# Optimization experiments

Measured on AMD Instinct MI355X. Metric: run time of the kernel, lower is better.

## Reference

```python
import jax, jax.numpy as jnp
import numpy as np

EMBED_DIM = 1024
HEAD_DIM = 128

def setup_inputs() -> dict:
    key = jax.random.key(0)
    ks = jax.random.split(key, 7)
    B, S = 4, 2048
    x = jax.random.normal(ks[0], (B, S, EMBED_DIM), dtype=jnp.float32)
    # Linear params: weight [embed_dim, head_dim] (applied as x @ W + b), scaled init
    scale = 1.0 / np.sqrt(EMBED_DIM)
    Wq = jax.random.normal(ks[1], (EMBED_DIM, HEAD_DIM), dtype=jnp.float32) * scale
    Wk = jax.random.normal(ks[2], (EMBED_DIM, HEAD_DIM), dtype=jnp.float32) * scale
    Wv = jax.random.normal(ks[3], (EMBED_DIM, HEAD_DIM), dtype=jnp.float32) * scale
    bq = jax.random.normal(ks[4], (HEAD_DIM,), dtype=jnp.float32) * 0.01
    bk = jax.random.normal(ks[5], (HEAD_DIM,), dtype=jnp.float32) * 0.01
    bv = jax.random.normal(ks[6], (HEAD_DIM,), dtype=jnp.float32) * 0.01
    return {"x": x, "Wq": Wq, "bq": bq, "Wk": Wk, "bk": bk, "Wv": Wv, "bv": bv}

def reference(x, Wq, bq, Wk, bk, Wv, bv):
    # x: [B, S, E]
    S = x.shape[1]
    norm = jnp.asarray(HEAD_DIM ** 0.5, x.dtype)
    q = x @ Wq + bq  # [B, S, D]
    k = x @ Wk + bk
    v = x @ Wv + bv
    scores = jnp.einsum('bsd,btd->bst', q, k) / norm  # [B, S, S]
    causal = jnp.tril(jnp.ones((S, S), dtype=bool))
    scores = jnp.where(causal, scores, -jnp.inf)
    att = jax.nn.softmax(scores, axis=-1)
    return jnp.einsum('bst,btd->bsd', att, v)  # [B, S, D]
```

## Files before the change

kernel.cpp:

```cpp
#include <hip/hip_runtime.h>
#include <hip/hip_bf16.h>

typedef __attribute__((ext_vector_type(8))) short short8;
typedef __attribute__((ext_vector_type(4))) float f32x4;

static __device__ __forceinline__ unsigned short f2bf(float f){
  union { float f; unsigned int u; } v; v.f = f;
  unsigned int r = v.u + 0x7fffu + ((v.u >> 16) & 1u);
  return (unsigned short)(r >> 16);
}

static __device__ __forceinline__ void load_lds16(const unsigned short* g, unsigned short* l){
  __builtin_amdgcn_global_load_lds(
      (const __attribute__((address_space(1))) unsigned int*)(g),
      (__attribute__((address_space(3))) unsigned int*)(l), 16, 0, 0);
}

__global__ void k_cvt_x(const float* __restrict__ x, unsigned short* __restrict__ xb){
  int i = (blockIdx.x * 256 + threadIdx.x) * 8;
  float4 a = *(const float4*)(x + i);
  float4 b = *(const float4*)(x + i + 4);
  unsigned short h[8];
  h[0]=f2bf(a.x); h[1]=f2bf(a.y); h[2]=f2bf(a.z); h[3]=f2bf(a.w);
  h[4]=f2bf(b.x); h[5]=f2bf(b.y); h[6]=f2bf(b.z); h[7]=f2bf(b.w);
  *(uint4*)(xb + i) = *(uint4*)h;
}

__global__ void k_prep_w(const float* __restrict__ Wq, const float* __restrict__ Wk,
                         const float* __restrict__ Wv,
                         const float* __restrict__ bq, const float* __restrict__ bk,
                         const float* __restrict__ bv,
                         unsigned short* __restrict__ Wt, float* __restrict__ bias){
  int gid = blockIdx.x * 256 + threadIdx.x;
  int p = gid >> 17;
  int rem = gid & 131071;
  int d = rem >> 10, e = rem & 1023;
  const float* W = (p==0) ? Wq : ((p==1) ? Wk : Wv);
  Wt[gid] = f2bf(W[e*128 + d]);
  if (gid < 384){
    int pp = gid >> 7, dd = gid & 127;
    bias[gid] = (pp==0) ? bq[dd] : ((pp==1) ? bk[dd] : bv[dd]);
  }
}

__global__ __launch_bounds__(256) void k_gemm_qkv(
    const unsigned short* __restrict__ Xb, const unsigned short* __restrict__ Wt,
    float* __restrict__ Cp){
  __shared__ __align__(16) unsigned short As[128*64];
  __shared__ __align__(16) unsigned short Bs[128*64];
  int tid = threadIdx.x;
  int m0 = blockIdx.x * 128;
  int p  = blockIdx.y;
  int kh = blockIdx.z;
  int w = tid >> 6, lane = tid & 63, quad = lane >> 4, l16 = lane & 15;
  int wm = (w >> 1) * 64, wn = (w & 1) * 64;
  f32x4 acc[4][4];
  #pragma unroll
  for (int i=0;i<4;i++)
    #pragma unroll
    for (int j=0;j<4;j++) acc[i][j] = (f32x4){0.f,0.f,0.f,0.f};

  const unsigned short* Wp = Wt + p * (128*1024);
  int rowbase = w * 32;
  const unsigned short* Ag = Xb + (m0 + rowbase + (lane>>3))*1024 + (lane&7)*8;
  const unsigned short* Bg = Wp + (rowbase + (lane>>3))*1024 + (lane&7)*8;
  unsigned short* Al = As + rowbase*64;
  unsigned short* Bl = Bs + rowbase*64;

  int kbeg = kh*512, kend = kbeg + 512;
  for (int k0 = kbeg; k0 < kend; k0 += 64){
    #pragma unroll
    for (int s8=0; s8<4; s8++){
      load_lds16(Ag + k0 + s8*8192, Al + s8*512);
      load_lds16(Bg + k0 + s8*8192, Bl + s8*512);
    }
    __syncthreads();
    #pragma unroll
    for (int kk=0; kk<64; kk+=32){
      short8 af[4], bf[4];
      #pragma unroll
      for (int i=0;i<4;i++) af[i] = *(const short8*)(As + (wm + i*16 + l16)*64 + kk + quad*8);
      #pragma unroll
      for (int j=0;j<4;j++) bf[j] = *(const short8*)(Bs + (wn + j*16 + l16)*64 + kk + quad*8);
      #pragma unroll
      for (int i=0;i<4;i++)
        #pragma unroll
        for (int j=0;j<4;j++)
          acc[i][j] = __builtin_amdgcn_mfma_f32_16x16x32_bf16(af[i], bf[j], acc[i][j], 0,0,0);
    }
    __syncthreads();
  }
  float* slot = Cp + (size_t)(((p*64 + blockIdx.x)*2 + kh)) * 16384;
  #pragma unroll
  for (int i=0;i<4;i++)
    #pragma unroll
    for (int j=0;j<4;j++)
      #pragma unroll
      for (int r=0;r<4;r++)
        slot[(wm + i*16 + quad*4 + r)*128 + wn + j*16 + l16] = acc[i][j][r];
}

__global__ __launch_bounds__(256) void k_gcomb(const float* __restrict__ Cp,
    const float* __restrict__ bias,
    unsigned short* __restrict__ Qsw, unsigned short* __restrict__ Ksw,
    unsigned short* __restrict__ Vsw){
  int mt = blockIdx.x, p = blockIdx.y, tid = threadIdx.x;
  const float* c0p = Cp + (size_t)((p*64+mt)*2) * 16384;
  const float* c1p = c0p + 16384;
  int m0 = mt*128;
  const float qscale = 0.08838834764831845f;
  if (p < 2){
    unsigned short* dst = (p==0)? Qsw : Ksw;
    float scale = (p==0)? qscale : 1.0f;
    for (int it=0; it<16; it++){
      int g = it*256 + tid;
      int row = g >> 5, cs = (g & 31)*4;
      f32x4 a = *(const f32x4*)(c0p + row*128 + cs);
      f32x4 bb = *(const f32x4*)(c1p + row*128 + cs);
      int grow = m0 + row;
      int rt = grow >> 4, m = grow & 15;
      int kc = cs >> 5, q2 = (cs >> 3) & 3, jj = cs & 7;
      unsigned short pk[4];
      #pragma unroll
      for (int k=0;k<4;k++) pk[k] = f2bf((a[k]+bb[k]+bias[p*128+cs+k])*scale);
      *(uint2*)(dst + rt*2048 + kc*512 + q2*128 + m*8 + jj) = *(uint2*)pk;
    }
  } else {
    for (int it=0; it<16; it++){
      int g = it*256 + tid;
      int col = g & 127, rg = g >> 7;
      int r0 = rg*4;
      float bv_ = bias[256 + col];
      unsigned short pk[4];
      #pragma unroll
      for (int k=0;k<4;k++){
        int row = r0 + k;
        pk[k] = f2bf(c0p[row*128+col] + c1p[row*128+col] + bv_);
      }
      int grow0 = m0 + r0;
      int bb2 = grow0 >> 11, s = grow0 & 2047;
      int t64 = s >> 6, srem = s & 63;
      int kc2 = srem >> 5, q2 = (srem >> 3) & 3, jj = srem & 7;
      int nt = col >> 4, l2 = col & 15;
      *(uint2*)(Vsw + (bb2*32+t64)*8192 + nt*1024 + kc2*512 + q2*128 + l2*8 + jj) = *(uint2*)pk;
    }
  }
}

__global__ __launch_bounds__(64) void k_attn(
    const unsigned short* __restrict__ Qsw, const unsigned short* __restrict__ Ksw,
    const unsigned short* __restrict__ Vsw, float* __restrict__ Apart){
  __shared__ __align__(16) unsigned short Pw[2*16*80];
  int x = blockIdx.x;
  int b = x & 3;
  int t = x >> 2;
  int c = t & 7;
  int qb = 63 - (t >> 3);
  int T32 = (qb >> 1) + 1;
  int nch = (T32 + 3) >> 2;
  if (c >= nch) return;
  int lane = threadIdx.x;
  int quad = lane >> 4, l16 = lane & 15;
  int q0 = qb * 32;

  short8 aq[2][4];
  #pragma unroll
  for (int s=0;s<2;s++)
    #pragma unroll
    for (int kc=0;kc<4;kc++)
      aq[s][kc] = *(const short8*)(Qsw + (b*128 + qb*2 + s)*2048 + kc*512 + lane*8);

  f32x4 o[2][8];
  #pragma unroll
  for (int s=0;s<2;s++)
    #pragma unroll
    for (int i=0;i<8;i++) o[s][i] = (f32x4){0.f,0.f,0.f,0.f};
  float mcol[2] = {-1e30f,-1e30f};
  float lcol[2] = {0.f,0.f};
  short8 ap[2][2];

  const unsigned short* Kb = Ksw + b*128*2048;
  const unsigned short* Vb = Vsw + b*32*8192;

  int tEnd = (T32 < c*4+4) ? T32 : (c*4+4);
  for (int tt = c*4; tt < tEnd; tt++){
    int t0 = tt * 64;
    f32x4 sc[2][4];
    #pragma unroll
    for (int s=0;s<2;s++)
      #pragma unroll
      for (int nt=0;nt<4;nt++) sc[s][nt] = (f32x4){0.f,0.f,0.f,0.f};
    #pragma unroll
    for (int nt=0;nt<4;nt++){
      const unsigned short* Kt = Kb + ((t0>>4)+nt)*2048 + lane*8;
      #pragma unroll
      for (int kc=0;kc<4;kc++){
        short8 kf = *(const short8*)(Kt + kc*512);
        sc[0][nt] = __builtin_amdgcn_mfma_f32_16x16x32_bf16(kf, aq[0][kc], sc[0][nt], 0,0,0);
        sc[1][nt] = __builtin_amdgcn_mfma_f32_16x16x32_bf16(kf, aq[1][kc], sc[1][nt], 0,0,0);
      }
    }
    #pragma unroll
    for (int s=0;s<2;s++){
      int qs = q0 + s*16;
      if (t0 + 63 > qs){
        #pragma unroll
        for (int nt=0;nt<4;nt++){
          int kb_ = t0 + nt*16 + quad*4;
          #pragma unroll
          for (int r=0;r<4;r++)
            if (kb_ + r > qs + l16) sc[s][nt][r] = -1e30f;
        }
      }
      float mt_ = -1e30f;
      #pragma unroll
      for (int nt=0;nt<4;nt++)
        #pragma unroll
        for (int r=0;r<4;r++) mt_ = fmaxf(mt_, sc[s][nt][r]);
      mt_ = fmaxf(mt_, __shfl_xor(mt_, 16));
      mt_ = fmaxf(mt_, __shfl_xor(mt_, 32));
      float mn = fmaxf(mcol[s], mt_);
      float al = __expf(mcol[s] - mn);
      mcol[s] = mn;
      float ls = 0.f;
      #pragma unroll
      for (int nt=0;nt<4;nt++)
        #pragma unroll
        for (int r=0;r<4;r++){
          float pv = __expf(sc[s][nt][r] - mn);
          sc[s][nt][r] = pv;
          ls += pv;
        }
      ls += __shfl_xor(ls, 16);
      ls += __shfl_xor(ls, 32);
      lcol[s] = lcol[s]*al + ls;
      #pragma unroll
      for (int r=0;r<4;r++){
        float ar = __shfl(al, quad*4 + r);
        #pragma unroll
        for (int nt=0;nt<8;nt++) o[s][nt][r] *= ar;
      }
      unsigned short* Pws = Pw + s*1280;
      #pragma unroll
      for (int nt=0;nt<4;nt++){
        unsigned short pk[4];
        #pragma unroll
        for (int r=0;r<4;r++) pk[r] = f2bf(sc[s][nt][r]);
        *(uint2*)(Pws + l16*80 + nt*16 + quad*4) = *(uint2*)pk;
      }
      ap[s][0] = *(const short8*)(Pws + l16*80 + quad*8);
      ap[s][1] = *(const short8*)(Pws + l16*80 + 32 + quad*8);
    }
    const unsigned short* Vt0 = Vb + (t0>>6)*8192 + lane*8;
    #pragma unroll
    for (int nt=0; nt<8; nt++)
      #pragma unroll
      for (int kc2=0;kc2<2;kc2++){
        short8 vf = *(const short8*)(Vt0 + nt*1024 + kc2*512);
        o[0][nt] = __builtin_amdgcn_mfma_f32_16x16x32_bf16(ap[0][kc2], vf, o[0][nt], 0,0,0);
        o[1][nt] = __builtin_amdgcn_mfma_f32_16x16x32_bf16(ap[1][kc2], vf, o[1][nt], 0,0,0);
      }
  }

  float* slot = Apart + (size_t)(((b*64 + qb)*8 + c)) * 4160;
  #pragma unroll
  for (int s=0;s<2;s++){
    #pragma unroll
    for (int nt=0;nt<8;nt++)
      #pragma unroll
      for (int r=0;r<4;r++)
        slot[(s*16 + quad*4 + r)*128 + nt*16 + l16] = o[s][nt][r];
    if (quad == 0){
      slot[4096 + s*16 + l16] = mcol[s];
      slot[4128 + s*16 + l16] = lcol[s];
    }
  }
}

__global__ __launch_bounds__(256) void k_acomb(const float* __restrict__ Apart,
                                               float* __restrict__ out){
  int b = blockIdx.x & 3, qb = blockIdx.x >> 2;
  int T32 = (qb >> 1) + 1;
  int nch = (T32 + 3) >> 2;
  const float* base = Apart + (size_t)((b*64 + qb)*8) * 4160;
  int tid = threadIdx.x;
  int row = tid >> 3;
  int c0 = (tid & 7) * 16;
  float m = -1e30f;
  for (int c=0;c<nch;c++) m = fmaxf(m, base[c*4160 + 4096 + row]);
  f32x4 acc[4];
  #pragma unroll
  for (int g=0;g<4;g++) acc[g] = (f32x4){0.f,0.f,0.f,0.f};
  float lsum = 0.f;
  for (int c=0;c<nch;c++){
    float e = __expf(base[c*4160 + 4096 + row] - m);
    lsum += base[c*4160 + 4128 + row] * e;
    #pragma unroll
    for (int g=0;g<4;g++){
      f32x4 v = *(const f32x4*)(base + c*4160 + row*128 + c0 + g*4);
      acc[g] += v * e;
    }
  }
  float inv = 1.0f / lsum;
  float* op = out + (size_t)(b*2048 + qb*32 + row)*128 + c0;
  #pragma unroll
  for (int g=0;g<4;g++){
    f32x4 r = acc[g] * inv;
    *(f32x4*)(op + g*4) = r;
  }
}

extern "C" void kernel_launch(void* const* d_in, const int* in_sizes, int n_in,
                              void* d_out, int out_size, void* d_ws, size_t ws_size,
                              hipStream_t stream) {
  const float* x  = (const float*)d_in[0];
  const float* Wq = (const float*)d_in[1];
  const float* bq = (const float*)d_in[2];
  const float* Wk = (const float*)d_in[3];
  const float* bk = (const float*)d_in[4];
  const float* Wv = (const float*)d_in[5];
  const float* bv = (const float*)d_in[6];
  char* ws = (char*)d_ws;
  unsigned short* Xb   = (unsigned short*)(ws);
  unsigned short* Wt   = (unsigned short*)(ws + 16777216);
  float*          bias = (float*)(ws + 17563648);
  unsigned short* Qsw  = (unsigned short*)(ws + 17565184);
  unsigned short* Ksw  = (unsigned short*)(ws + 19662336);
  unsigned short* Vsw  = (unsigned short*)(ws + 21759488);
  float*          Cp   = (float*)(ws + 23856640);
  float*          Apart= (float*)(ws + 49022464);
  float* out = (float*)d_out;

  hipLaunchKernelGGL(k_cvt_x,   dim3(4096),    dim3(256), 0, stream, x, Xb);
  hipLaunchKernelGGL(k_prep_w,  dim3(1536),    dim3(256), 0, stream, Wq, Wk, Wv, bq, bk, bv, Wt, bias);
  hipLaunchKernelGGL(k_gemm_qkv,dim3(64,3,2),  dim3(256), 0, stream, Xb, Wt, Cp);
  hipLaunchKernelGGL(k_gcomb,   dim3(64,3),    dim3(256), 0, stream, Cp, bias, Qsw, Ksw, Vsw);
  hipLaunchKernelGGL(k_attn,    dim3(2048),    dim3(64),  0, stream, Qsw, Ksw, Vsw, Apart);
  hipLaunchKernelGGL(k_acomb,   dim3(256),     dim3(256), 0, stream, Apart, out);
}
```

Measured before the change: 139.7 us.

## Fuse QKV GEMM epilogue, drop split-K, store attention partials in bf16

The QKV projection GEMM now uses 64-row tiles over the full K range without split-K. It applies bias, scaling and the swizzled bf16 stores directly in its epilogue, which removes the fp32 partial buffer and the separate combine kernel. Attention partial outputs are written as bf16 in a lane-ordered layout, and the combine kernel reads them with the new indexing, roughly halving that traffic. In exchange the GEMM has less K-parallelism per block, and the combine step loses some precision and now does strided scalar bf16 loads.

```diff
diff --git a/kernel.cpp b/kernel.cpp
--- a/kernel.cpp
+++ b/kernel.cpp
@@ -8,6 +8,9 @@
   union { float f; unsigned int u; } v; v.f = f;
   unsigned int r = v.u + 0x7fffu + ((v.u >> 16) & 1u);
   return (unsigned short)(r >> 16);
+}
+static __device__ __forceinline__ float bf2f(unsigned short u){
+  union { unsigned int u; float f; } v; v.u = ((unsigned int)u) << 16; return v.f;
 }
 
 static __device__ __forceinline__ void load_lds16(const unsigned short* g, unsigned short* l){
@@ -45,111 +48,93 @@
 
 __global__ __launch_bounds__(256) void k_gemm_qkv(
     const unsigned short* __restrict__ Xb, const unsigned short* __restrict__ Wt,
-    float* __restrict__ Cp){
-  __shared__ __align__(16) unsigned short As[128*64];
-  __shared__ __align__(16) unsigned short Bs[128*64];
-  int tid = threadIdx.x;
-  int m0 = blockIdx.x * 128;
-  int p  = blockIdx.y;
-  int kh = blockIdx.z;
-  int w = tid >> 6, lane = tid & 63, quad = lane >> 4, l16 = lane & 15;
-  int wm = (w >> 1) * 64, wn = (w & 1) * 64;
-  f32x4 acc[4][4];
-  #pragma unroll
-  for (int i=0;i<4;i++)
-    #pragma unroll
-    for (int j=0;j<4;j++) acc[i][j] = (f32x4){0.f,0.f,0.f,0.f};
-
-  const unsigned short* Wp = Wt + p * (128*1024);
-  int rowbase = w * 32;
-  const unsigned short* Ag = Xb + (m0 + rowbase + (lane>>3))*1024 + (lane&7)*8;
-  const unsigned short* Bg = Wp + (rowbase + (lane>>3))*1024 + (lane&7)*8;
-  unsigned short* Al = As + rowbase*64;
-  unsigned short* Bl = Bs + rowbase*64;
-
-  int kbeg = kh*512, kend = kbeg + 512;
-  for (int k0 = kbeg; k0 < kend; k0 += 64){
-    #pragma unroll
-    for (int s8=0; s8<4; s8++){
-      load_lds16(Ag + k0 + s8*8192, Al + s8*512);
-      load_lds16(Bg + k0 + s8*8192, Bl + s8*512);
-    }
-    __syncthreads();
-    #pragma unroll
-    for (int kk=0; kk<64; kk+=32){
-      short8 af[4], bf[4];
-      #pragma unroll
-      for (int i=0;i<4;i++) af[i] = *(const short8*)(As + (wm + i*16 + l16)*64 + kk + quad*8);
-      #pragma unroll
-      for (int j=0;j<4;j++) bf[j] = *(const short8*)(Bs + (wn + j*16 + l16)*64 + kk + quad*8);
-      #pragma unroll
-      for (int i=0;i<4;i++)
-        #pragma unroll
-        for (int j=0;j<4;j++)
-          acc[i][j] = __builtin_amdgcn_mfma_f32_16x16x32_bf16(af[i], bf[j], acc[i][j], 0,0,0);
-    }
-    __syncthreads();
-  }
-  float* slot = Cp + (size_t)(((p*64 + blockIdx.x)*2 + kh)) * 16384;
-  #pragma unroll
-  for (int i=0;i<4;i++)
-    #pragma unroll
-    for (int j=0;j<4;j++)
-      #pragma unroll
-      for (int r=0;r<4;r++)
-        slot[(wm + i*16 + quad*4 + r)*128 + wn + j*16 + l16] = acc[i][j][r];
-}
-
-__global__ __launch_bounds__(256) void k_gcomb(const float* __restrict__ Cp,
     const float* __restrict__ bias,
     unsigned short* __restrict__ Qsw, unsigned short* __restrict__ Ksw,
     unsigned short* __restrict__ Vsw){
-  int mt = blockIdx.x, p = blockIdx.y, tid = threadIdx.x;
-  const float* c0p = Cp + (size_t)((p*64+mt)*2) * 16384;
-  const float* c1p = c0p + 16384;
-  int m0 = mt*128;
+  __shared__ __align__(16) unsigned short As[64*64];
+  __shared__ __align__(16) unsigned short Bs[128*64];
+  int tid = threadIdx.x;
+  int m0 = blockIdx.x * 64;
+  int p  = blockIdx.y;
+  int w = tid >> 6, lane = tid & 63, quad = lane >> 4, l16 = lane & 15;
+  int wm = (w & 1) * 32, wn = (w >> 1) * 64;
+  f32x4 acc[2][4];
+  #pragma unroll
+  for (int i=0;i<2;i++)
+    #pragma unroll
+    for (int j=0;j<4;j++) acc[i][j] = (f32x4){0.f,0.f,0.f,0.f};
+
+  const unsigned short* Wp = Wt + p * (128*1024);
+  const unsigned short* Ag = Xb + (m0 + w*16 + (lane>>3))*1024 + (lane&7)*8;
+  const unsigned short* Bg = Wp + (w*32 + (lane>>3))*1024 + (lane&7)*8;
+  unsigned short* Al = As + w*16*64;
+  unsigned short* Bl = Bs + w*32*64;
+
+  for (int k0 = 0; k0 < 1024; k0 += 64){
+    load_lds16(Ag + k0,        Al);
+    load_lds16(Ag + k0 + 8192, Al + 512);
+    #pragma unroll
+    for (int s=0; s<4; s++)
+      load_lds16(Bg + k0 + s*8192, Bl + s*512);
+    __syncthreads();
+    #pragma unroll
+    for (int kk=0; kk<64; kk+=32){
+      short8 af[2], bf[4];
+      #pragma unroll
+      for (int i=0;i<2;i++) af[i] = *(const short8*)(As + (wm + i*16 + l16)*64 + kk + quad*8);
+      #pragma unroll
+      for (int j=0;j<4;j++) bf[j] = *(const short8*)(Bs + (wn + j*16 + l16)*64 + kk + quad*8);
+      #pragma unroll
+      for (int i=0;i<2;i++)
+        #pragma unroll
+        for (int j=0;j<4;j++)
+          acc[i][j] = __builtin_amdgcn_mfma_f32_16x16x32_bf16(af[i], bf[j], acc[i][j], 0,0,0);
+    }
+    __syncthreads();
+  }
   const float qscale = 0.08838834764831845f;
   if (p < 2){
     unsigned short* dst = (p==0)? Qsw : Ksw;
     float scale = (p==0)? qscale : 1.0f;
-    for (int it=0; it<16; it++){
-      int g = it*256 + tid;
-      int row = g >> 5, cs = (g & 31)*4;
-      f32x4 a = *(const f32x4*)(c0p + row*128 + cs);
-      f32x4 bb = *(const f32x4*)(c1p + row*128 + cs);
-      int grow = m0 + row;
-      int rt = grow >> 4, m = grow & 15;
-      int kc = cs >> 5, q2 = (cs >> 3) & 3, jj = cs & 7;
-      unsigned short pk[4];
-      #pragma unroll
-      for (int k=0;k<4;k++) pk[k] = f2bf((a[k]+bb[k]+bias[p*128+cs+k])*scale);
-      *(uint2*)(dst + rt*2048 + kc*512 + q2*128 + m*8 + jj) = *(uint2*)pk;
+    #pragma unroll
+    for (int i=0;i<2;i++){
+      #pragma unroll
+      for (int j=0;j<4;j++){
+        int col = wn + j*16 + l16;
+        float bv_ = bias[p*128 + col];
+        int kc = col >> 5, q2 = (col >> 3) & 3, jj = col & 7;
+        #pragma unroll
+        for (int r=0;r<4;r++){
+          int row = m0 + wm + i*16 + quad*4 + r;
+          int rt = row >> 4, m = row & 15;
+          dst[rt*2048 + kc*512 + q2*128 + m*8 + jj] = f2bf((acc[i][j][r] + bv_)*scale);
+        }
+      }
     }
   } else {
-    for (int it=0; it<16; it++){
-      int g = it*256 + tid;
-      int col = g & 127, rg = g >> 7;
-      int r0 = rg*4;
-      float bv_ = bias[256 + col];
-      unsigned short pk[4];
-      #pragma unroll
-      for (int k=0;k<4;k++){
-        int row = r0 + k;
-        pk[k] = f2bf(c0p[row*128+col] + c1p[row*128+col] + bv_);
-      }
-      int grow0 = m0 + r0;
-      int bb2 = grow0 >> 11, s = grow0 & 2047;
+    #pragma unroll
+    for (int i=0;i<2;i++){
+      int row0 = m0 + wm + i*16 + quad*4;
+      int bb = row0 >> 11, s = row0 & 2047;
       int t64 = s >> 6, srem = s & 63;
-      int kc2 = srem >> 5, q2 = (srem >> 3) & 3, jj = srem & 7;
-      int nt = col >> 4, l2 = col & 15;
-      *(uint2*)(Vsw + (bb2*32+t64)*8192 + nt*1024 + kc2*512 + q2*128 + l2*8 + jj) = *(uint2*)pk;
+      int kc2 = srem >> 5, q2v = (srem >> 3) & 3, jjb = srem & 7;
+      #pragma unroll
+      for (int j=0;j<4;j++){
+        int col = wn + j*16 + l16;
+        float bv_ = bias[256 + col];
+        int nt = (wn + j*16) >> 4;
+        unsigned short pk[4];
+        #pragma unroll
+        for (int r=0;r<4;r++) pk[r] = f2bf(acc[i][j][r] + bv_);
+        *(uint2*)(Vsw + (bb*32+t64)*8192 + nt*1024 + kc2*512 + q2v*128 + l16*8 + jjb) = *(uint2*)pk;
+      }
     }
   }
 }
 
 __global__ __launch_bounds__(64) void k_attn(
     const unsigned short* __restrict__ Qsw, const unsigned short* __restrict__ Ksw,
-    const unsigned short* __restrict__ Vsw, float* __restrict__ Apart){
+    const unsigned short* __restrict__ Vsw, unsigned short* __restrict__ Apart){
   __shared__ __align__(16) unsigned short Pw[2*16*80];
   int x = blockIdx.x;
   int b = x & 3;
@@ -262,51 +247,62 @@
       }
   }
 
-  float* slot = Apart + (size_t)(((b*64 + qb)*8 + c)) * 4160;
-  #pragma unroll
-  for (int s=0;s<2;s++){
-    #pragma unroll
-    for (int nt=0;nt<8;nt++)
-      #pragma unroll
-      for (int r=0;r<4;r++)
-        slot[(s*16 + quad*4 + r)*128 + nt*16 + l16] = o[s][nt][r];
-    if (quad == 0){
-      slot[4096 + s*16 + l16] = mcol[s];
-      slot[4128 + s*16 + l16] = lcol[s];
-    }
-  }
-}
-
-__global__ __launch_bounds__(256) void k_acomb(const float* __restrict__ Apart,
+  unsigned short* slot = Apart + (size_t)(((b*64 + qb)*8 + c)) * 4224;
+  #pragma unroll
+  for (int s=0;s<2;s++)
+    #pragma unroll
+    for (int nt=0;nt<8;nt++){
+      unsigned short pk[4];
+      #pragma unroll
+      for (int r=0;r<4;r++) pk[r] = f2bf(o[s][nt][r]);
+      *(uint2*)(slot + (s*8+nt)*256 + lane*4) = *(uint2*)pk;
+    }
+  float* fslot = (float*)(slot + 4096);
+  if (quad == 0){
+    #pragma unroll
+    for (int s=0;s<2;s++){
+      fslot[s*16 + l16]      = mcol[s];
+      fslot[32 + s*16 + l16] = lcol[s];
+    }
+  }
+}
+
+__global__ __launch_bounds__(256) void k_acomb(const unsigned short* __restrict__ Apart,
                                                float* __restrict__ out){
   int b = blockIdx.x & 3, qb = blockIdx.x >> 2;
   int T32 = (qb >> 1) + 1;
   int nch = (T32 + 3) >> 2;
-  const float* base = Apart + (size_t)((b*64 + qb)*8) * 4160;
+  const unsigned short* slot0 = Apart + (size_t)((b*64 + qb)*8) * 4224;
   int tid = threadIdx.x;
   int row = tid >> 3;
   int c0 = (tid & 7) * 16;
+  int s = row >> 4, qrow = row & 15;
+  int quad = qrow >> 2, r = qrow & 3;
+  int nt = c0 >> 4;
   float m = -1e30f;
-  for (int c=0;c<nch;c++) m = fmaxf(m, base[c*4160 + 4096 + row]);
-  f32x4 acc[4];
-  #pragma unroll
-  for (int g=0;g<4;g++) acc[g] = (f32x4){0.f,0.f,0.f,0.f};
+  for (int c=0;c<nch;c++){
+    const float* fs = (const float*)(slot0 + c*4224 + 4096);
+    m = fmaxf(m, fs[s*16 + qrow]);
+  }
+  float acc[16];
+  #pragma unroll
+  for (int k=0;k<16;k++) acc[k] = 0.f;
   float lsum = 0.f;
   for (int c=0;c<nch;c++){
-    float e = __expf(base[c*4160 + 4096 + row] - m);
-    lsum += base[c*4160 + 4128 + row] * e;
-    #pragma unroll
-    for (int g=0;g<4;g++){
-      f32x4 v = *(const f32x4*)(base + c*4160 + row*128 + c0 + g*4);
-      acc[g] += v * e;
-    }
+    const float* fs = (const float*)(slot0 + c*4224 + 4096);
+    float e = __expf(fs[s*16 + qrow] - m);
+    lsum += fs[32 + s*16 + qrow] * e;
+    const unsigned short* ob = slot0 + c*4224 + (s*8+nt)*256 + quad*64 + r;
+    #pragma unroll
+    for (int k=0;k<16;k++)
+      acc[k] += bf2f(ob[k*4]) * e;
   }
   float inv = 1.0f / lsum;
   float* op = out + (size_t)(b*2048 + qb*32 + row)*128 + c0;
   #pragma unroll
   for (int g=0;g<4;g++){
-    f32x4 r = acc[g] * inv;
-    *(f32x4*)(op + g*4) = r;
+    float4 rv = {acc[g*4]*inv, acc[g*4+1]*inv, acc[g*4+2]*inv, acc[g*4+3]*inv};
+    *(float4*)(op + g*4) = rv;
   }
 }
 
@@ -327,14 +323,12 @@
   unsigned short* Qsw  = (unsigned short*)(ws + 17565184);
   unsigned short* Ksw  = (unsigned short*)(ws + 19662336);
   unsigned short* Vsw  = (unsigned short*)(ws + 21759488);
-  float*          Cp   = (float*)(ws + 23856640);
-  float*          Apart= (float*)(ws + 49022464);
+  unsigned short* Apart= (unsigned short*)(ws + 23856640);
   float* out = (float*)d_out;
 
   hipLaunchKernelGGL(k_cvt_x,   dim3(4096),    dim3(256), 0, stream, x, Xb);
   hipLaunchKernelGGL(k_prep_w,  dim3(1536),    dim3(256), 0, stream, Wq, Wk, Wv, bq, bk, bv, Wt, bias);
-  hipLaunchKernelGGL(k_gemm_qkv,dim3(64,3,2),  dim3(256), 0, stream, Xb, Wt, Cp);
-  hipLaunchKernelGGL(k_gcomb,   dim3(64,3),    dim3(256), 0, stream, Cp, bias, Qsw, Ksw, Vsw);
+  hipLaunchKernelGGL(k_gemm_qkv,dim3(128,3),   dim3(256), 0, stream, Xb, Wt, bias, Qsw, Ksw, Vsw);
   hipLaunchKernelGGL(k_attn,    dim3(2048),    dim3(64),  0, stream, Qsw, Ksw, Vsw, Apart);
   hipLaunchKernelGGL(k_acomb,   dim3(256),     dim3(256), 0, stream, Apart, out);
 }
```

Result: no change. 141.6 us (+1.3%).
